# Kernel optimization log

Hardware: AMD Instinct MI355X
Metric: run time of the kernel (lower is better)

## Reference

```python
import jax, jax.numpy as jnp
import numpy as np

N = 255  # 17 * time_input(15) graph nodes


def spmm(rows, cols, vals, x):
    """Batched sparse (COO) @ dense: x is [B, N, F] -> [B, N, F]."""
    g = x[:, cols, :] * vals[None, :, None]                      # [B, nnz, F]
    out = jax.ops.segment_sum(jnp.swapaxes(g, 0, 1), rows,
                              num_segments=N)                     # [N, B, F]
    return jnp.swapaxes(out, 0, 1)


def setup_inputs() -> dict:
    key = jax.random.key(0)
    ks = jax.random.split(key, 32)
    B, nnz = 256, 2040
    inp = {"H": jax.random.normal(ks[0], (B, N, 2), jnp.float32)}
    for i, nm in enumerate(["sm_s", "sm_t", "sp_s", "sp_t"]):
        inp[nm + "_rows"] = jax.random.randint(ks[1 + 3 * i], (nnz,), 0, N, jnp.int32)
        inp[nm + "_cols"] = jax.random.randint(ks[2 + 3 * i], (nnz,), 0, N, jnp.int32)
        inp[nm + "_vals"] = jax.random.uniform(ks[3 + 3 * i], (nnz,), jnp.float32)
    dims = [(2, 400), (400, 300), (300, 100), (100, 300), (300, 400), (400, 2)]
    wnames = ["W0", "W1", "W2", "Wd0", "Wd1", "Wd2"]
    for j, (di, do) in enumerate(dims):
        inp[wnames[j]] = jax.random.normal(ks[13 + j], (di, do), jnp.float32) / np.sqrt(di).astype(np.float32)
        inp["b" + wnames[j][1:]] = jnp.zeros((do,), jnp.float32)
    return inp


def reference(H, sm_s_rows, sm_s_cols, sm_s_vals,
              sm_t_rows, sm_t_cols, sm_t_vals,
              sp_s_rows, sp_s_cols, sp_s_vals,
              sp_t_rows, sp_t_cols, sp_t_vals,
              W0, b0, W1, b1, W2, b2, Wd0, bd0, Wd1, bd1, Wd2, bd2):
    def layer(x, W, b, r, c, v):
        # Dense projection fused with Laplacian SpMM + ReLU (same math as the
        # per-sample Python loop in the original, batched over B).
        return jax.nn.relu(spmm(r, c, v, x @ W + b))

    # encoder: Laplacian smoothing (enc0, enc1 with s_DADsm; enc2 with t_DADsm)
    H = layer(H, W0, b0, sm_s_rows, sm_s_cols, sm_s_vals)
    H = layer(H, W1, b1, sm_s_rows, sm_s_cols, sm_s_vals)
    H = layer(H, W2, b2, sm_t_rows, sm_t_cols, sm_t_vals)
    # decoder: Laplacian sharpening (dec0 with t_DADsp; dec1, dec2 with s_DADsp)
    H = layer(H, Wd0, bd0, sp_t_rows, sp_t_cols, sp_t_vals)
    H = layer(H, Wd1, bd1, sp_s_rows, sp_s_cols, sp_s_vals)
    H = layer(H, Wd2, bd2, sp_s_rows, sp_s_cols, sp_s_vals)
    return H  # [B, 255, 2]
```

## Files before the change

### kernel.cpp

```cpp
#include <hip/hip_runtime.h>
#include <hip/hip_bf16.h>


#define NN 255
#define YCH 2048

typedef __attribute__((ext_vector_type(8))) short short8;
typedef __attribute__((ext_vector_type(4))) float floatx4;

__device__ __forceinline__ float bf2f(ushort u) {
    union { uint u; float f; } c; c.u = ((uint)u) << 16; return c.f;
}
__device__ __forceinline__ ushort f2bf(float f) {
    union { float f; uint u; } c; c.f = f;
    uint u = c.u + 0x7fff + ((c.u >> 16) & 1);
    return (ushort)(u >> 16);
}
__device__ __forceinline__ short8 u4_frag(uint4 v) {
    union { uint4 u; short8 s; } c; c.u = v; return c.s;
}
__device__ __forceinline__ void gl_lds16(const ushort* g, ushort* l) {
    __builtin_amdgcn_global_load_lds(
        (const __attribute__((address_space(1))) void*)g,
        (__attribute__((address_space(3))) void*)l, 16, 0, 0);
}

__global__ void zero_k(int* p, int n) {
    int i = blockIdx.x * blockDim.x + threadIdx.x;
    if (i < n) p[i] = 0;
}

__global__ void edge_k(const int* __restrict__ r0, const int* __restrict__ c0, const float* __restrict__ v0,
                       const int* __restrict__ r1, const int* __restrict__ c1, const float* __restrict__ v1,
                       const int* __restrict__ r2, const int* __restrict__ c2, const float* __restrict__ v2,
                       const int* __restrict__ r3, const int* __restrict__ c3, const float* __restrict__ v3,
                       float* Sd, float* rs, int nnz) {
    int gi = blockIdx.y;
    int e = blockIdx.x * blockDim.x + threadIdx.x;
    if (e >= nnz) return;
    const int* rr = gi == 0 ? r0 : gi == 1 ? r1 : gi == 2 ? r2 : r3;
    const int* cc = gi == 0 ? c0 : gi == 1 ? c1 : gi == 2 ? c2 : c3;
    const float* vv = gi == 0 ? v0 : gi == 1 ? v1 : gi == 2 ? v2 : v3;
    int r = rr[e], c = cc[e];
    float v = vv[e];
    atomicAdd(&Sd[gi * 65536 + r * 256 + c], v);
    atomicAdd(&rs[gi * 256 + r], v);
}

__device__ __forceinline__ void wpiece(const float* __restrict__ W, ushort* __restrict__ Wt,
                                       int K, int N, int Kpad, int idx) {
    int n = idx / Kpad, k = idx - n * Kpad;
    float v = (n < N && k < K) ? W[(size_t)k * N + n] : 0.f;
    Wt[idx] = f2bf(v);
}

__global__ void conv_k(const float* __restrict__ Sd, ushort* __restrict__ Sb,
                       const float* __restrict__ W1, ushort* __restrict__ Wt1,
                       const float* __restrict__ W2, ushort* __restrict__ Wt2,
                       const float* __restrict__ W3, ushort* __restrict__ Wt3,
                       const float* __restrict__ W4, ushort* __restrict__ Wt4) {
    int idx = blockIdx.x * blockDim.x + threadIdx.x;
    if (idx < 262144) { Sb[idx] = f2bf(Sd[idx]); return; }
    idx -= 262144;
    if (idx < 133120) { wpiece(W1, Wt1, 400, 300, 416, idx); return; }
    idx -= 133120;
    if (idx < 40960)  { wpiece(W2, Wt2, 300, 100, 320, idx); return; }
    idx -= 40960;
    if (idx < 40960)  { wpiece(W3, Wt3, 100, 300, 128, idx); return; }
    idx -= 40960;
    if (idx < 143360) { wpiece(W4, Wt4, 300, 400, 320, idx); }
}

__global__ __launch_bounds__(256) void l0_fused(const float* __restrict__ H,
                                                const float* __restrict__ Sd0,
                                                const float* __restrict__ W0,
                                                const float* __restrict__ b0,
                                                const float* __restrict__ rs0,
                                                ushort* __restrict__ Y) {
    __shared__ float hsh[512];
    __shared__ float ssh[512];
    int b = blockIdx.x, t = threadIdx.x;
    if (t < NN) {
        hsh[t * 2]     = H[((size_t)b * NN + t) * 2];
        hsh[t * 2 + 1] = H[((size_t)b * NN + t) * 2 + 1];
    } else {
        hsh[t * 2] = 0.f; hsh[t * 2 + 1] = 0.f;
    }
    __syncthreads();
    const float4* Sr = (const float4*)(Sd0 + (size_t)t * 256);
    float s0 = 0.f, s1 = 0.f;
    #pragma unroll 8
    for (int c4 = 0; c4 < 64; ++c4) {
        float4 v = Sr[c4];
        const float2* hp = (const float2*)&hsh[c4 * 8];
        float2 h0 = hp[0], h1 = hp[1], h2 = hp[2], h3 = hp[3];
        s0 = fmaf(v.x, h0.x, s0); s1 = fmaf(v.x, h0.y, s1);
        s0 = fmaf(v.y, h1.x, s0); s1 = fmaf(v.y, h1.y, s1);
        s0 = fmaf(v.z, h2.x, s0); s1 = fmaf(v.z, h2.y, s1);
        s0 = fmaf(v.w, h3.x, s0); s1 = fmaf(v.w, h3.y, s1);
    }
    ssh[t * 2] = s0; ssh[t * 2 + 1] = s1;
    __syncthreads();
    uint* out = (uint*)(Y + (((size_t)b) << 8) * 416);
    for (int i = 0; i < 200; ++i) {
        int idx = i * 256 + t;
        int m = idx / 200, n2 = idx - m * 200;
        int n = n2 * 2;
        float x0 = ssh[m * 2], x1 = ssh[m * 2 + 1];
        float rsm = rs0[m];
        float y0 = fmaf(x0, W0[n],     fmaf(x1, W0[400 + n],     rsm * b0[n]));
        float y1 = fmaf(x0, W0[n + 1], fmaf(x1, W0[400 + n + 1], rsm * b0[n + 1]));
        out[(size_t)m * 208 + n2] =
            (uint)f2bf(fmaxf(y0, 0.f)) | ((uint)f2bf(fmaxf(y1, 0.f)) << 16);
    }
}

__global__ __launch_bounds__(256, 3) void fused_layer(const ushort* __restrict__ X,
                                                      const ushort* __restrict__ Wt,
                                                      const ushort* __restrict__ Sg,
                                                      const float* __restrict__ bias,
                                                      ushort* __restrict__ Z,
                                                      int Kpad, int Nfeat, int FsN,
                                                      int nft) {
    __shared__ ushort smem[22528];
    ushort* As0 = smem;
    ushort* As1 = smem + 2048;
    ushort* As2 = smem + 4096;
    ushort* Bs0 = smem + 6144;
    ushort* Bs1 = smem + 14336;
    ushort* Ys  = smem;

    int li = blockIdx.x;
    int x = li & 7, rr = li >> 3;
    int ft = rr % nft, b = (rr / nft) * 8 + x;
    int f0 = ft * 64;

    int t = threadIdx.x;
    int w = t >> 6, lane = t & 63;
    int frow = lane & 15, quad = lane >> 4;
    int rot = ((quad + (frow >> 2)) & 3) * 8;

    const ushort* Xb = X + (((size_t)b) << 8) * (size_t)Kpad;
    const ushort* gB0 = Xb + (size_t)(64 * w +  0 + (lane >> 2)) * Kpad + (lane & 3) * 8;
    const ushort* gB1 = Xb + (size_t)(64 * w + 16 + (lane >> 2)) * Kpad + (lane & 3) * 8;
    const ushort* gB2 = Xb + (size_t)(64 * w + 32 + (lane >> 2)) * Kpad + (lane & 3) * 8;
    const ushort* gB3 = Xb + (size_t)(64 * w + 48 + (lane >> 2)) * Kpad + (lane & 3) * 8;
    const ushort* gA  = Wt + (size_t)(f0 + 16 * w + (lane >> 2)) * Kpad + (lane & 3) * 8;

    floatx4 acc[4][4];
    #pragma unroll
    for (int i = 0; i < 4; ++i)
        #pragma unroll
        for (int j = 0; j < 4; ++j) acc[i][j] = (floatx4)0.f;

    int nk1 = Kpad >> 5;

    {
        ushort* Bd = Bs0 + w * 2048;
        gl_lds16(gB0, Bd);        gl_lds16(gB1, Bd + 512);
        gl_lds16(gB2, Bd + 1024); gl_lds16(gB3, Bd + 1536);
        gl_lds16(gA,  As0 + w * 512);
        ushort* Bd1 = Bs1 + w * 2048;
        gl_lds16(gB0 + 32, Bd1);        gl_lds16(gB1 + 32, Bd1 + 512);
        gl_lds16(gB2 + 32, Bd1 + 1024); gl_lds16(gB3 + 32, Bd1 + 1536);
        gl_lds16(gA  + 32, As1 + w * 512);
    }
    __builtin_amdgcn_sched_barrier(0);
    asm volatile("s_waitcnt vmcnt(5)" ::: "memory");
    __builtin_amdgcn_s_barrier();
    __builtin_amdgcn_sched_barrier(0);

    ushort *a0 = As0, *a1 = As1, *a2 = As2;
    ushort *bc = Bs0, *bn = Bs1;

    for (int ks = 0; ks < nk1; ++ks) {
        const ushort* Ab = a0 + frow * 32 + quad * 8;
        const ushort* Bb = bc + (w * 64 + frow) * 32 + quad * 8;
        short8 xf[4], wf[4];
        #pragma unroll
        for (int i = 0; i < 4; ++i) {
            xf[i] = u4_frag(*(const uint4*)(Bb + i * 512));
            wf[i] = u4_frag(*(const uint4*)(Ab + i * 512));
        }
        asm volatile("s_waitcnt lgkmcnt(0)" ::: "memory");
        __builtin_amdgcn_sched_barrier(0);
        if (ks + 2 < nk1) {
            int off = (ks + 2) * 32;
            ushort* Bd = bc + w * 2048;
            gl_lds16(gB0 + off, Bd);        gl_lds16(gB1 + off, Bd + 512);
            gl_lds16(gB2 + off, Bd + 1024); gl_lds16(gB3 + off, Bd + 1536);
            gl_lds16(gA  + off, a2 + w * 512);
        }
        #pragma unroll
        for (int i = 0; i < 4; ++i)
            #pragma unroll
            for (int j = 0; j < 4; ++j)
                acc[i][j] = __builtin_amdgcn_mfma_f32_16x16x32_bf16(xf[i], wf[j], acc[i][j], 0, 0, 0);
        __builtin_amdgcn_sched_barrier(0);
        if (ks + 2 < nk1)
            asm volatile("s_waitcnt vmcnt(5)" ::: "memory");
        else
            asm volatile("s_waitcnt vmcnt(0)" ::: "memory");
        __builtin_amdgcn_s_barrier();
        __builtin_amdgcn_sched_barrier(0);
        ushort* ta = a0; a0 = a1; a1 = a2; a2 = ta;
        ushort* tb = bc; bc = bn; bn = tb;
    }

    const ushort* Sp = Sg + (size_t)(w * 64 + frow) * 256 + quad * 8;
    uint4 ps[4];
    #pragma unroll
    for (int i = 0; i < 4; ++i) ps[i] = *(const uint4*)(Sp + i * 4096);

    #pragma unroll
    for (int j = 0; j < 4; ++j) {
        int f = j * 16 + frow;
        float bv = (f0 + f < Nfeat) ? bias[f0 + f] : 0.f;
        #pragma unroll
        for (int i = 0; i < 4; ++i) {
            int chunk = 2 * w + (i >> 1);
            int gc = 2 * (i & 1) + (quad >> 1);
            int base = chunk * YCH + f * 32 + (((gc + (frow >> 2)) & 3) * 8) + (quad & 1) * 4;
            uint lo = (uint)f2bf(acc[i][j][0] + bv) | ((uint)f2bf(acc[i][j][1] + bv) << 16);
            uint hi = (uint)f2bf(acc[i][j][2] + bv) | ((uint)f2bf(acc[i][j][3] + bv) << 16);
            *(uint2*)(&Ys[base]) = make_uint2(lo, hi);
        }
    }
    __syncthreads();

    #pragma unroll
    for (int i = 0; i < 4; ++i)
        #pragma unroll
        for (int j = 0; j < 4; ++j) acc[i][j] = (floatx4)0.f;

    for (int ks = 0; ks < 8; ++ks) {
        uint4 pn[4];
        if (ks < 7) {
            #pragma unroll
            for (int i = 0; i < 4; ++i)
                pn[i] = *(const uint4*)(Sp + i * 4096 + (ks + 1) * 32);
        }
        short8 bf[4];
        #pragma unroll
        for (int j = 0; j < 4; ++j)
            bf[j] = u4_frag(*(const uint4*)(&Ys[ks * YCH + (j * 16 + frow) * 32 + rot]));
        #pragma unroll
        for (int i = 0; i < 4; ++i) {
            short8 af = u4_frag(ps[i]);
            #pragma unroll
            for (int j = 0; j < 4; ++j)
                acc[i][j] = __builtin_amdgcn_mfma_f32_16x16x32_bf16(af, bf[j], acc[i][j], 0, 0, 0);
        }
        #pragma unroll
        for (int i = 0; i < 4; ++i) ps[i] = pn[i];
    }

    #pragma unroll
    for (int i = 0; i < 4; ++i)
        #pragma unroll
        for (int r = 0; r < 4; ++r) {
            int rg = w * 64 + i * 16 + quad * 4 + r;
            ushort* Zr = Z + (size_t)((b << 8) + rg) * FsN + f0;
            #pragma unroll
            for (int j = 0; j < 4; ++j)
                Zr[j * 16 + frow] = f2bf(fmaxf(acc[i][j][r], 0.f));
        }
}

__global__ __launch_bounds__(256) void l5_fused(const ushort* __restrict__ X,
                                                const float* __restrict__ Sd2,
                                                const float* __restrict__ Wd2,
                                                const float* __restrict__ bd2,
                                                float* __restrict__ out) {
    __shared__ float ysh[512];
    int b = blockIdx.x, t = threadIdx.x;
    const uint4* Xr = (const uint4*)(X + ((size_t)((b << 8) + t)) * 448);
    const float4* Wp = (const float4*)Wd2;
    float a0 = bd2[0], a1 = bd2[1];
    for (int i = 0; i < 50; ++i) {
        uint4 p = Xr[i];
        uint pv[4] = {p.x, p.y, p.z, p.w};
        #pragma unroll
        for (int q = 0; q < 4; ++q) {
            float x0 = bf2f((ushort)(pv[q] & 0xffffu));
            float x1 = bf2f((ushort)(pv[q] >> 16));
            float4 w = Wp[i * 4 + q];
            a0 = fmaf(x0, w.x, a0); a1 = fmaf(x0, w.y, a1);
            a0 = fmaf(x1, w.z, a0); a1 = fmaf(x1, w.w, a1);
        }
    }
    ysh[t * 2] = a0; ysh[t * 2 + 1] = a1;
    __syncthreads();
    if (t < NN) {
        const float4* Sr = (const float4*)(Sd2 + (size_t)t * 256);
        float s0 = 0.f, s1 = 0.f;
        #pragma unroll 8
        for (int c4 = 0; c4 < 64; ++c4) {
            float4 v = Sr[c4];
            const float2* yp = (const float2*)&ysh[c4 * 8];
            float2 y0 = yp[0], y1 = yp[1], y2 = yp[2], y3 = yp[3];
            s0 = fmaf(v.x, y0.x, s0); s1 = fmaf(v.x, y0.y, s1);
            s0 = fmaf(v.y, y1.x, s0); s1 = fmaf(v.y, y1.y, s1);
            s0 = fmaf(v.z, y2.x, s0); s1 = fmaf(v.z, y2.y, s1);
            s0 = fmaf(v.w, y3.x, s0); s1 = fmaf(v.w, y3.y, s1);
        }
        out[((size_t)b * NN + t) * 2]     = fmaxf(s0, 0.f);
        out[((size_t)b * NN + t) * 2 + 1] = fmaxf(s1, 0.f);
    }
}

extern "C" void kernel_launch(void* const* d_in, const int* in_sizes, int n_in,
                              void* d_out, int out_size, void* d_ws, size_t ws_size,
                              hipStream_t stream) {
    const float* H = (const float*)d_in[0];
    const int*   g_rows[4] = {(const int*)d_in[1], (const int*)d_in[4], (const int*)d_in[7], (const int*)d_in[10]};
    const int*   g_cols[4] = {(const int*)d_in[2], (const int*)d_in[5], (const int*)d_in[8], (const int*)d_in[11]};
    const float* g_vals[4] = {(const float*)d_in[3], (const float*)d_in[6], (const float*)d_in[9], (const float*)d_in[12]};
    const float* W0  = (const float*)d_in[13]; const float* b0  = (const float*)d_in[14];
    const float* W1  = (const float*)d_in[15]; const float* b1  = (const float*)d_in[16];
    const float* W2  = (const float*)d_in[17]; const float* b2  = (const float*)d_in[18];
    const float* Wd0 = (const float*)d_in[19]; const float* bd0 = (const float*)d_in[20];
    const float* Wd1 = (const float*)d_in[21]; const float* bd1 = (const float*)d_in[22];
    const float* Wd2 = (const float*)d_in[23]; const float* bd2 = (const float*)d_in[24];
    float* out = (float*)d_out;

    const int nnz = in_sizes[1];
    const int B   = in_sizes[0] / (NN * 2);
    const int Mp  = B * 256;

    ushort* bufA = (ushort*)d_ws;
    ushort* bufB = bufA + (size_t)Mp * 448;
    ushort* Wt1 = bufB + (size_t)Mp * 320;
    ushort* Wt2 = Wt1 + 320 * 416;
    ushort* Wt3 = Wt2 + 128 * 320;
    ushort* Wt4 = Wt3 + 320 * 128;
    ushort* Sb  = Wt4 + 448 * 320;
    float*  rs  = (float*)(Sb + 4 * 65536);
    float*  Sd  = rs + 4 * 256;
    const int ZN = 4 * 256 + 4 * 65536;

    zero_k<<<(ZN + 255) / 256, 256, 0, stream>>>((int*)rs, ZN);
    edge_k<<<dim3((nnz + 255) / 256, 4), 256, 0, stream>>>(
        g_rows[0], g_cols[0], g_vals[0], g_rows[1], g_cols[1], g_vals[1],
        g_rows[2], g_cols[2], g_vals[2], g_rows[3], g_cols[3], g_vals[3],
        Sd, rs, nnz);
    conv_k<<<(620544 + 255) / 256, 256, 0, stream>>>(Sd, Sb, W1, Wt1, W2, Wt2, Wd0, Wt3, Wd1, Wt4);

    l0_fused<<<B, 256, 0, stream>>>(H, Sd + 0 * 65536, W0, b0, rs + 0, bufA);

    fused_layer<<<B * 5, 256, 0, stream>>>(bufA, Wt1, Sb + 0 * 65536, b1, bufB, 416, 300, 320, 5);
    fused_layer<<<B * 2, 256, 0, stream>>>(bufB, Wt2, Sb + 1 * 65536, b2, bufA, 320, 100, 128, 2);
    fused_layer<<<B * 5, 256, 0, stream>>>(bufA, Wt3, Sb + 3 * 65536, bd0, bufB, 128, 300, 320, 5);
    fused_layer<<<B * 7, 256, 0, stream>>>(bufB, Wt4, Sb + 2 * 65536, bd1, bufA, 320, 400, 448, 7);

    l5_fused<<<B, 256, 0, stream>>>(bufA, Sd + 2 * 65536, Wd2, bd2, out);
}
```

Measured before the change: 342.1 us.

## Give each wave private copies of weight tiles to drop per-step block barriers

Result: slower. 359.2 us (+5.0%).

```diff
diff --git a/kernel.cpp b/kernel.cpp
--- a/kernel.cpp
+++ b/kernel.cpp
@@ -115,19 +115,18 @@
     }
 }
 
-__global__ __launch_bounds__(256, 3) void fused_layer(const ushort* __restrict__ X,
+__global__ __launch_bounds__(256, 2) void fused_layer(const ushort* __restrict__ X,
                                                       const ushort* __restrict__ Wt,
                                                       const ushort* __restrict__ Sg,
                                                       const float* __restrict__ bias,
                                                       ushort* __restrict__ Z,
                                                       int Kpad, int Nfeat, int FsN,
                                                       int nft) {
-    __shared__ ushort smem[22528];
+    __shared__ __align__(16) ushort smem[32768];
     ushort* As0 = smem;
-    ushort* As1 = smem + 2048;
-    ushort* As2 = smem + 4096;
-    ushort* Bs0 = smem + 6144;
-    ushort* Bs1 = smem + 14336;
+    ushort* As1 = smem + 8192;
+    ushort* Bs0 = smem + 16384;
+    ushort* Bs1 = smem + 24576;
     ushort* Ys  = smem;
 
     int li = blockIdx.x;
@@ -145,7 +144,15 @@
     const ushort* gB1 = Xb + (size_t)(64 * w + 16 + (lane >> 2)) * Kpad + (lane & 3) * 8;
     const ushort* gB2 = Xb + (size_t)(64 * w + 32 + (lane >> 2)) * Kpad + (lane & 3) * 8;
     const ushort* gB3 = Xb + (size_t)(64 * w + 48 + (lane >> 2)) * Kpad + (lane & 3) * 8;
-    const ushort* gA  = Wt + (size_t)(f0 + 16 * w + (lane >> 2)) * Kpad + (lane & 3) * 8;
+    const ushort* gA0 = Wt + (size_t)(f0 +  0 + (lane >> 2)) * Kpad + (lane & 3) * 8;
+    const ushort* gA1 = gA0 + 16 * (size_t)Kpad;
+    const ushort* gA2 = gA0 + 32 * (size_t)Kpad;
+    const ushort* gA3 = gA0 + 48 * (size_t)Kpad;
+
+    ushort* AsW0 = As0 + w * 2048;
+    ushort* AsW1 = As1 + w * 2048;
+    ushort* BsW0 = Bs0 + w * 2048;
+    ushort* BsW1 = Bs1 + w * 2048;
 
     floatx4 acc[4][4];
     #pragma unroll
@@ -155,27 +162,23 @@
 
     int nk1 = Kpad >> 5;
 
-    {
-        ushort* Bd = Bs0 + w * 2048;
-        gl_lds16(gB0, Bd);        gl_lds16(gB1, Bd + 512);
-        gl_lds16(gB2, Bd + 1024); gl_lds16(gB3, Bd + 1536);
-        gl_lds16(gA,  As0 + w * 512);
-        ushort* Bd1 = Bs1 + w * 2048;
-        gl_lds16(gB0 + 32, Bd1);        gl_lds16(gB1 + 32, Bd1 + 512);
-        gl_lds16(gB2 + 32, Bd1 + 1024); gl_lds16(gB3 + 32, Bd1 + 1536);
-        gl_lds16(gA  + 32, As1 + w * 512);
-    }
-    __builtin_amdgcn_sched_barrier(0);
-    asm volatile("s_waitcnt vmcnt(5)" ::: "memory");
-    __builtin_amdgcn_s_barrier();
-    __builtin_amdgcn_sched_barrier(0);
-
-    ushort *a0 = As0, *a1 = As1, *a2 = As2;
-    ushort *bc = Bs0, *bn = Bs1;
+    gl_lds16(gB0, BsW0);        gl_lds16(gB1, BsW0 + 512);
+    gl_lds16(gB2, BsW0 + 1024); gl_lds16(gB3, BsW0 + 1536);
+    gl_lds16(gA0, AsW0);        gl_lds16(gA1, AsW0 + 512);
+    gl_lds16(gA2, AsW0 + 1024); gl_lds16(gA3, AsW0 + 1536);
+    gl_lds16(gB0 + 32, BsW1);        gl_lds16(gB1 + 32, BsW1 + 512);
+    gl_lds16(gB2 + 32, BsW1 + 1024); gl_lds16(gB3 + 32, BsW1 + 1536);
+    gl_lds16(gA0 + 32, AsW1);        gl_lds16(gA1 + 32, AsW1 + 512);
+    gl_lds16(gA2 + 32, AsW1 + 1024); gl_lds16(gA3 + 32, AsW1 + 1536);
 
     for (int ks = 0; ks < nk1; ++ks) {
-        const ushort* Ab = a0 + frow * 32 + quad * 8;
-        const ushort* Bb = bc + (w * 64 + frow) * 32 + quad * 8;
+        if (ks + 1 < nk1)
+            asm volatile("s_waitcnt vmcnt(8)" ::: "memory");
+        else
+            asm volatile("s_waitcnt vmcnt(0)" ::: "memory");
+        __builtin_amdgcn_sched_barrier(0);
+        const ushort* Ab = ((ks & 1) ? As1 : As0) + w * 2048 + frow * 32 + quad * 8;
+        const ushort* Bb = ((ks & 1) ? Bs1 : Bs0) + w * 2048 + frow * 32 + quad * 8;
         short8 xf[4], wf[4];
         #pragma unroll
         for (int i = 0; i < 4; ++i) {
@@ -186,31 +189,26 @@
         __builtin_amdgcn_sched_barrier(0);
         if (ks + 2 < nk1) {
             int off = (ks + 2) * 32;
-            ushort* Bd = bc + w * 2048;
+            ushort* Ad = (ks & 1) ? AsW1 : AsW0;
+            ushort* Bd = (ks & 1) ? BsW1 : BsW0;
             gl_lds16(gB0 + off, Bd);        gl_lds16(gB1 + off, Bd + 512);
             gl_lds16(gB2 + off, Bd + 1024); gl_lds16(gB3 + off, Bd + 1536);
-            gl_lds16(gA  + off, a2 + w * 512);
+            gl_lds16(gA0 + off, Ad);        gl_lds16(gA1 + off, Ad + 512);
+            gl_lds16(gA2 + off, Ad + 1024); gl_lds16(gA3 + off, Ad + 1536);
         }
         #pragma unroll
         for (int i = 0; i < 4; ++i)
             #pragma unroll
             for (int j = 0; j < 4; ++j)
                 acc[i][j] = __builtin_amdgcn_mfma_f32_16x16x32_bf16(xf[i], wf[j], acc[i][j], 0, 0, 0);
-        __builtin_amdgcn_sched_barrier(0);
-        if (ks + 2 < nk1)
-            asm volatile("s_waitcnt vmcnt(5)" ::: "memory");
-        else
-            asm volatile("s_waitcnt vmcnt(0)" ::: "memory");
-        __builtin_amdgcn_s_barrier();
-        __builtin_amdgcn_sched_barrier(0);
-        ushort* ta = a0; a0 = a1; a1 = a2; a2 = ta;
-        ushort* tb = bc; bc = bn; bn = tb;
     }
 
     const ushort* Sp = Sg + (size_t)(w * 64 + frow) * 256 + quad * 8;
     uint4 ps[4];
     #pragma unroll
     for (int i = 0; i < 4; ++i) ps[i] = *(const uint4*)(Sp + i * 4096);
+
+    __syncthreads();
 
     #pragma unroll
     for (int j = 0; j < 4; ++j) {
```
